# Optimization experiments

Hardware: AMD Instinct MI355X
Metric: run time of the kernel (lower is better)

## Reference

```python
import jax, jax.numpy as jnp
import numpy as np

N, E, G = 50000, 800000, 512
IN_CH, HID, HEADS, OUT_CH, LAYERS = 128, 32, 8, 1, 3
NEG_SLOPE = 0.2  # PyG GATConv default


def gat_conv(x, src, dst, W, a_src, a_dst, bias):
    # x: [N, F_in]; W: [F_in, H*C]; a_src/a_dst: [H, C]; bias: [H*C]
    h = (x @ W).reshape(N, HEADS, HID)                     # [N, H, C]
    alpha_src = jnp.einsum('nhc,hc->nh', h, a_src)          # [N, H]
    alpha_dst = jnp.einsum('nhc,hc->nh', h, a_dst)          # [N, H]
    e = jax.nn.leaky_relu(alpha_src[src] + alpha_dst[dst], NEG_SLOPE)  # [E', H]
    # segment softmax over incoming edges of each destination node
    m = jax.ops.segment_max(e, dst, num_segments=N)
    m = jnp.where(jnp.isfinite(m), m, 0.0)
    ex = jnp.exp(e - m[dst])
    denom = jax.ops.segment_sum(ex, dst, num_segments=N)
    alpha = ex / (denom[dst] + 1e-16)                       # [E', H]
    msg = h[src] * alpha[:, :, None]                        # [E', H, C]
    out = jax.ops.segment_sum(msg, dst, num_segments=N)     # [N, H, C]
    return out.reshape(N, HEADS * HID) + bias


def setup_inputs() -> dict:
    key = jax.random.key(0)
    ks = jax.random.split(key, 20)
    inp = {}
    inp['x'] = jax.random.normal(ks[0], (N, IN_CH), dtype=jnp.float32)
    inp['edge_index'] = jax.random.randint(ks[1], (2, E), 0, N, dtype=jnp.int64)
    inp['batch'] = jnp.sort(jax.random.randint(ks[2], (N,), 0, G, dtype=jnp.int64))
    fan_ins = [IN_CH, HEADS * HID, HEADS * HID]
    for l in range(LAYERS):
        s = (2.0 / fan_ins[l]) ** 0.5
        inp[f'W{l}'] = jax.random.normal(ks[3 + 4 * l], (fan_ins[l], HEADS * HID), dtype=jnp.float32) * s
        inp[f'a_src{l}'] = jax.random.normal(ks[4 + 4 * l], (HEADS, HID), dtype=jnp.float32) * 0.1
        inp[f'a_dst{l}'] = jax.random.normal(ks[5 + 4 * l], (HEADS, HID), dtype=jnp.float32) * 0.1
        inp[f'bias{l}'] = jnp.zeros((HEADS * HID,), dtype=jnp.float32)
    inp['lin_w'] = jax.random.normal(ks[15], (HEADS * HID, OUT_CH), dtype=jnp.float32) * 0.06
    inp['lin_b'] = jnp.zeros((OUT_CH,), dtype=jnp.float32)
    return inp


def reference(x, edge_index, batch,
              W0, a_src0, a_dst0, bias0,
              W1, a_src1, a_dst1, bias1,
              W2, a_src2, a_dst2, bias2,
              lin_w, lin_b):
    # add self-loops (GATConv default add_self_loops=True)
    loop = jnp.arange(N, dtype=edge_index.dtype)
    src = jnp.concatenate([edge_index[0], loop])
    dst = jnp.concatenate([edge_index[1], loop])
    params = [(W0, a_src0, a_dst0, bias0), (W1, a_src1, a_dst1, bias1), (W2, a_src2, a_dst2, bias2)]
    h = x
    for (W, a_s, a_d, b) in params:
        h = gat_conv(h, src, dst, W, a_s, a_d, b)
        h = jax.nn.elu(h)
        # dropout is identity in eval mode
    # global mean pool over graphs
    sums = jax.ops.segment_sum(h, batch, num_segments=G)           # [G, H*C]
    cnts = jax.ops.segment_sum(jnp.ones((N,), h.dtype), batch, num_segments=G)
    pooled = sums / jnp.maximum(cnts, 1.0)[:, None]
    return pooled @ lin_w + lin_b                                   # [G, OUT_CH]
```

## Files before the change

### kernel.cpp

```cpp
#include <hip/hip_runtime.h>

#define HC 256
#define HEADS 8
#define HID 32
#define GRAPHS 512
#define NEG_SLOPE 0.2f

typedef __bf16 bf16x8 __attribute__((ext_vector_type(8)));
typedef float f32x4 __attribute__((ext_vector_type(4)));

__device__ __forceinline__ unsigned short f2bf(float x) {
    unsigned u = __float_as_uint(x);
    return (unsigned short)((u + 0x7fffu + ((u >> 16) & 1u)) >> 16);
}
__device__ __forceinline__ float bf2f(unsigned short b) {
    return __uint_as_float(((unsigned)b) << 16);
}

__device__ __forceinline__ int IDX(const void* p, long long i, int mode) {
    if (mode) return (int)((const long long*)p)[i];
    return ((const int*)p)[i];
}

__global__ void detect_kernel(const unsigned int* __restrict__ words, int* __restrict__ mode, int e) {
    __shared__ unsigned int red[256];
    unsigned int v = 0;
    int lim = e < 4096 ? e : 4096;
    for (int i = threadIdx.x; i < lim; i += 256) v |= words[2 * i + 1];
    red[threadIdx.x] = v;
    __syncthreads();
    for (int off = 128; off > 0; off >>= 1) {
        if (threadIdx.x < off) red[threadIdx.x] |= red[threadIdx.x + off];
        __syncthreads();
    }
    if (threadIdx.x == 0) *mode = (red[0] == 0u) ? 1 : 0;
}

__global__ void hist_kernel(const void* __restrict__ edge, const int* __restrict__ mode,
                            int* __restrict__ hist, int e) {
    int m = mode[0];
    int i = blockIdx.x * blockDim.x + threadIdx.x;
    if (i < e) atomicAdd(&hist[IDX(edge, (long long)e + i, m)], 1);
}

__global__ void scan1(const int* __restrict__ hist, int* __restrict__ excl,
                      int* __restrict__ bsum, int n) {
    __shared__ int buf[256];
    int i = blockIdx.x * 256 + threadIdx.x;
    int v = (i < n) ? hist[i] : 0;
    buf[threadIdx.x] = v;
    __syncthreads();
    for (int off = 1; off < 256; off <<= 1) {
        int t = (threadIdx.x >= (unsigned)off) ? buf[threadIdx.x - off] : 0;
        __syncthreads();
        buf[threadIdx.x] += t;
        __syncthreads();
    }
    if (i < n) excl[i] = buf[threadIdx.x] - v;
    if (threadIdx.x == 255) bsum[blockIdx.x] = buf[255];
}

__global__ void scan2(int* __restrict__ bsum, int nb) {
    __shared__ int buf[256];
    int v = (threadIdx.x < (unsigned)nb) ? bsum[threadIdx.x] : 0;
    buf[threadIdx.x] = v;
    __syncthreads();
    for (int off = 1; off < 256; off <<= 1) {
        int t = (threadIdx.x >= (unsigned)off) ? buf[threadIdx.x - off] : 0;
        __syncthreads();
        buf[threadIdx.x] += t;
        __syncthreads();
    }
    if (threadIdx.x < (unsigned)nb) bsum[threadIdx.x] = buf[threadIdx.x] - v;
}

__global__ void scan3(int* __restrict__ row_ptr, const int* __restrict__ bsum, int n, int e) {
    int i = blockIdx.x * 256 + threadIdx.x;
    if (i < n) row_ptr[i] += bsum[i >> 8];
    if (i == 0) row_ptr[n] = e;
}

__global__ void scatter_kernel(const void* __restrict__ edge, const int* __restrict__ mode,
                               const int* __restrict__ row_ptr, int* __restrict__ fill,
                               int* __restrict__ outs, int* __restrict__ outd, int e) {
    int m = mode[0];
    int i = blockIdx.x * blockDim.x + threadIdx.x;
    if (i < e) {
        int d = IDX(edge, (long long)e + i, m);
        int pos = row_ptr[d] + atomicAdd(&fill[d], 1);
        outs[pos] = IDX(edge, (long long)i, m);
        outd[pos] = d;
    }
}

__global__ void cast_kernel(const float* __restrict__ x, unsigned short* __restrict__ xb,
                            int nquad) {
    int i = blockIdx.x * blockDim.x + threadIdx.x;
    if (i >= nquad) return;
    float4 v = *(const float4*)(x + (size_t)i * 4);
    ushort4 u = {f2bf(v.x), f2bf(v.y), f2bf(v.z), f2bf(v.w)};
    *(ushort4*)(xb + (size_t)i * 4) = u;
}

__global__ void wtrans_kernel(const float* __restrict__ W, unsigned short* __restrict__ Wt,
                              int K) {
    int idx = blockIdx.x * blockDim.x + threadIdx.x;
    if (idx >= 256 * K) return;
    int c = idx / K, k = idx - c * K;
    Wt[idx] = f2bf(W[(size_t)k * 256 + c]);
}

__global__ __launch_bounds__(256) void gemm_mfma(const unsigned short* __restrict__ A,
                                                 const unsigned short* __restrict__ Wt,
                                                 unsigned short* __restrict__ Cb,
                                                 int M, int K) {
    __shared__ unsigned short Ab[64][40];
    __shared__ unsigned short Bt[128][40];
    const int tid = threadIdx.x;
    const int wave = tid >> 6, lane = tid & 63;
    const int wr = wave >> 1, wc = wave & 1;
    const int row0 = blockIdx.x * 64, col0 = blockIdx.y * 128;
    const int r4 = tid >> 2, q = tid & 3;
    const int l15 = lane & 15, g8 = (lane >> 4) * 8;
    f32x4 acc[2][4] = {};

    for (int k0 = 0; k0 < K; k0 += 32) {
        int ar = row0 + r4;
        ar = ar < M ? ar : M - 1;
        *(uint4*)&Ab[r4][q * 8] = *(const uint4*)&A[(size_t)ar * K + k0 + q * 8];
#pragma unroll
        for (int h = 0; h < 2; ++h) {
            int br = r4 + h * 64;
            *(uint4*)&Bt[br][q * 8] = *(const uint4*)&Wt[(size_t)(col0 + br) * K + k0 + q * 8];
        }
        __syncthreads();
        bf16x8 af[2], bfr[4];
#pragma unroll
        for (int i = 0; i < 2; ++i) af[i] = *(const bf16x8*)&Ab[wr * 32 + i * 16 + l15][g8];
#pragma unroll
        for (int j = 0; j < 4; ++j) bfr[j] = *(const bf16x8*)&Bt[wc * 64 + j * 16 + l15][g8];
#pragma unroll
        for (int i = 0; i < 2; ++i)
#pragma unroll
            for (int j = 0; j < 4; ++j)
                acc[i][j] = __builtin_amdgcn_mfma_f32_16x16x32_bf16(af[i], bfr[j], acc[i][j],
                                                                    0, 0, 0);
        __syncthreads();
    }
    const int g = lane >> 4;
#pragma unroll
    for (int i = 0; i < 2; ++i) {
#pragma unroll
        for (int r = 0; r < 4; ++r) {
            int row = row0 + wr * 32 + i * 16 + g * 4 + r;
            if (row < M) {
#pragma unroll
                for (int j = 0; j < 4; ++j) {
                    int col = col0 + wc * 64 + j * 16 + l15;
                    Cb[(size_t)row * HC + col] = f2bf(acc[i][j][r]);
                }
            }
        }
    }
}

__global__ void alpha_kernel(const unsigned short* __restrict__ h,
                             const float* __restrict__ a_src,
                             const float* __restrict__ a_dst, float* __restrict__ asrc,
                             float* __restrict__ adst, int n) {
    int t = blockIdx.x * blockDim.x + threadIdx.x;
    if (t >= n * HEADS) return;
    int node = t >> 3, head = t & 7;
    const ushort4* hp = (const ushort4*)(h + (size_t)node * HC + head * HID);
    const float4* w1 = (const float4*)(a_src + head * HID);
    const float4* w2 = (const float4*)(a_dst + head * HID);
    float s1 = 0.f, s2 = 0.f;
#pragma unroll
    for (int q = 0; q < 8; ++q) {
        ushort4 hv = hp[q];
        float4 a1 = w1[q], a2 = w2[q];
        float h0 = bf2f(hv.x), h1 = bf2f(hv.y), h2 = bf2f(hv.z), h3 = bf2f(hv.w);
        s1 += h0 * a1.x + h1 * a1.y + h2 * a1.z + h3 * a1.w;
        s2 += h0 * a2.x + h1 * a2.y + h2 * a2.z + h3 * a2.w;
    }
    asrc[t] = s1;
    adst[t] = s2;
}

__global__ void wexp_kernel(const int* __restrict__ srcs, const int* __restrict__ dsts,
                            const float* __restrict__ asrc, const float* __restrict__ adst,
                            float* __restrict__ wexp, int e) {
    int i = blockIdx.x * blockDim.x + threadIdx.x;
    if (i >= e) return;
    int s = srcs[i], d = dsts[i];
    float4 s0 = *(const float4*)(asrc + (size_t)s * 8);
    float4 s1 = *(const float4*)(asrc + (size_t)s * 8 + 4);
    float4 d0 = *(const float4*)(adst + (size_t)d * 8);
    float4 d1 = *(const float4*)(adst + (size_t)d * 8 + 4);
    float v[8] = {s0.x + d0.x, s0.y + d0.y, s0.z + d0.z, s0.w + d0.w,
                  s1.x + d1.x, s1.y + d1.y, s1.z + d1.z, s1.w + d1.w};
#pragma unroll
    for (int q = 0; q < 8; ++q) {
        float t = v[q] > 0.f ? v[q] : NEG_SLOPE * v[q];
        v[q] = __expf(fminf(t, 75.f));
    }
    *(float4*)(wexp + (size_t)i * 8) = make_float4(v[0], v[1], v[2], v[3]);
    *(float4*)(wexp + (size_t)i * 8 + 4) = make_float4(v[4], v[5], v[6], v[7]);
}

#define ACC_EDGE(gv, wv)                                                      \
    do {                                                                      \
        unsigned _u0 = gv.x, _u1 = gv.y, _u2 = gv.z, _u3 = gv.w;              \
        acc[0] = fmaf(wv, __uint_as_float(_u0 << 16), acc[0]);                \
        acc[1] = fmaf(wv, __uint_as_float(_u0 & 0xffff0000u), acc[1]);        \
        acc[2] = fmaf(wv, __uint_as_float(_u1 << 16), acc[2]);                \
        acc[3] = fmaf(wv, __uint_as_float(_u1 & 0xffff0000u), acc[3]);        \
        acc[4] = fmaf(wv, __uint_as_float(_u2 << 16), acc[4]);                \
        acc[5] = fmaf(wv, __uint_as_float(_u2 & 0xffff0000u), acc[5]);        \
        acc[6] = fmaf(wv, __uint_as_float(_u3 << 16), acc[6]);                \
        acc[7] = fmaf(wv, __uint_as_float(_u3 & 0xffff0000u), acc[7]);        \
    } while (0)

template <bool LAST>
__global__ __launch_bounds__(256) void gat_aggregate(
    const unsigned short* __restrict__ hb, const float* __restrict__ wexp,
    const float* __restrict__ asrc, const float* __restrict__ adst,
    const int* __restrict__ row_ptr, const int* __restrict__ srcs,
    const float* __restrict__ bias, unsigned short* __restrict__ out16,
    const void* __restrict__ batch, const int* __restrict__ mode,
    const float* __restrict__ lin_w, float* __restrict__ gsum,
    float* __restrict__ gcnt, int n) {
    const int lane = threadIdx.x & 63;
    const int half = lane >> 5;
    const int l32 = lane & 31;
    int wid = (int)((blockIdx.x * blockDim.x + threadIdx.x) >> 6);
    int node = wid * 2 + half;
    if (node >= n) return;
    const int head = l32 >> 2;
    const int c0 = l32 * 8;
    const int beg = row_ptr[node], end = row_ptr[node + 1];

    float e0 = asrc[node * 8 + head] + adst[node * 8 + head];
    e0 = e0 > 0.f ? e0 : NEG_SLOPE * e0;
    float w0 = __expf(fminf(e0, 75.f));
    float denom = w0;
    float acc[8] = {};
    {
        uint4 g = *(const uint4*)(hb + (size_t)node * HC + c0);
        ACC_EDGE(g, w0);
    }
    int j = beg;
    for (; j + 4 <= end; j += 4) {
        int s0 = srcs[j], s1 = srcs[j + 1], s2 = srcs[j + 2], s3 = srcs[j + 3];
        uint4 g0 = *(const uint4*)(hb + (size_t)s0 * HC + c0);
        uint4 g1 = *(const uint4*)(hb + (size_t)s1 * HC + c0);
        uint4 g2 = *(const uint4*)(hb + (size_t)s2 * HC + c0);
        uint4 g3 = *(const uint4*)(hb + (size_t)s3 * HC + c0);
        float x0 = wexp[(size_t)(j + 0) * 8 + head];
        float x1 = wexp[(size_t)(j + 1) * 8 + head];
        float x2 = wexp[(size_t)(j + 2) * 8 + head];
        float x3 = wexp[(size_t)(j + 3) * 8 + head];
        denom += x0 + x1 + x2 + x3;
        ACC_EDGE(g0, x0);
        ACC_EDGE(g1, x1);
        ACC_EDGE(g2, x2);
        ACC_EDGE(g3, x3);
    }
    for (; j < end; ++j) {
        int s = srcs[j];
        uint4 g = *(const uint4*)(hb + (size_t)s * HC + c0);
        float x = wexp[(size_t)j * 8 + head];
        denom += x;
        ACC_EDGE(g, x);
    }

    const float invd = 1.f / (denom + 1e-16f);
    float4 b0 = *(const float4*)(bias + c0);
    float4 b1 = *(const float4*)(bias + c0 + 4);
    float o[8] = {fmaf(acc[0], invd, b0.x), fmaf(acc[1], invd, b0.y),
                  fmaf(acc[2], invd, b0.z), fmaf(acc[3], invd, b0.w),
                  fmaf(acc[4], invd, b1.x), fmaf(acc[5], invd, b1.y),
                  fmaf(acc[6], invd, b1.z), fmaf(acc[7], invd, b1.w)};
#pragma unroll
    for (int q = 0; q < 8; ++q) o[q] = o[q] > 0.f ? o[q] : __expf(o[q]) - 1.f;
    if (!LAST) {
        uint4 u;
        u.x = (unsigned)f2bf(o[0]) | ((unsigned)f2bf(o[1]) << 16);
        u.y = (unsigned)f2bf(o[2]) | ((unsigned)f2bf(o[3]) << 16);
        u.z = (unsigned)f2bf(o[4]) | ((unsigned)f2bf(o[5]) << 16);
        u.w = (unsigned)f2bf(o[6]) | ((unsigned)f2bf(o[7]) << 16);
        *(uint4*)(out16 + (size_t)node * HC + c0) = u;
    } else {
        float4 wA = *(const float4*)(lin_w + c0);
        float4 wB = *(const float4*)(lin_w + c0 + 4);
        float p = o[0] * wA.x + o[1] * wA.y + o[2] * wA.z + o[3] * wA.w +
                  o[4] * wB.x + o[5] * wB.y + o[6] * wB.z + o[7] * wB.w;
#pragma unroll
        for (int off = 1; off <= 16; off <<= 1) p += __shfl_xor(p, off, 64);
        if (l32 == 0) {
            int g = IDX(batch, node, mode[0]);
            atomicAdd(&gsum[g], p);
            atomicAdd(&gcnt[g], 1.f);
        }
    }
}

__global__ void final_kernel(const float* __restrict__ gsum, const float* __restrict__ gcnt,
                             const float* __restrict__ lin_b, float* __restrict__ outp) {
    int g = blockIdx.x * blockDim.x + threadIdx.x;
    if (g >= GRAPHS) return;
    float c = gcnt[g];
    c = c > 1.f ? c : 1.f;
    outp[g] = gsum[g] / c + lin_b[0];
}

extern "C" void kernel_launch(void* const* d_in, const int* in_sizes, int n_in,
                              void* d_out, int out_size, void* d_ws, size_t ws_size,
                              hipStream_t stream) {
    const float* x = (const float*)d_in[0];
    const void* edge = d_in[1];
    const void* batch = d_in[2];
    const float* W[3]    = {(const float*)d_in[3], (const float*)d_in[7],  (const float*)d_in[11]};
    const float* ASRC[3] = {(const float*)d_in[4], (const float*)d_in[8],  (const float*)d_in[12]};
    const float* ADST[3] = {(const float*)d_in[5], (const float*)d_in[9],  (const float*)d_in[13]};
    const float* BIAS[3] = {(const float*)d_in[6], (const float*)d_in[10], (const float*)d_in[14]};
    const float* lin_w = (const float*)d_in[15];
    const float* lin_b = (const float*)d_in[16];
    float* outp = (float*)d_out;

    const int n = in_sizes[0] / 128;
    const int e = in_sizes[1] / 2;
    const int IN_CH = 128;

    char* ws = (char*)d_ws;
    size_t off = 0;
    auto alloc = [&](size_t bytes) -> void* {
        void* p = ws + off;
        off = (off + bytes + 255) & ~(size_t)255;
        return p;
    };
    unsigned short* xb   = (unsigned short*)alloc((size_t)n * IN_CH * 2);
    unsigned short* hb16 = (unsigned short*)alloc((size_t)n * HC * 2);
    unsigned short* gb16 = (unsigned short*)alloc((size_t)n * HC * 2);
    unsigned short* wt0  = (unsigned short*)alloc((size_t)256 * IN_CH * 2);
    unsigned short* wt1  = (unsigned short*)alloc((size_t)256 * HC * 2);
    unsigned short* wt2  = (unsigned short*)alloc((size_t)256 * HC * 2);
    float* as_buf = (float*)alloc((size_t)n * HEADS * 4);
    float* ad_buf = (float*)alloc((size_t)n * HEADS * 4);
    int* hist     = (int*)alloc((size_t)n * 4);
    int* row_ptr  = (int*)alloc((size_t)(n + 1) * 4);
    int* bsum     = (int*)alloc(1024);
    int* mode     = (int*)alloc(256);
    int* srcs     = (int*)alloc((size_t)e * 4);
    int* dsts     = (int*)alloc((size_t)e * 4);
    float* wexp   = (float*)alloc((size_t)e * HEADS * 4);
    float* gsum   = (float*)alloc((size_t)GRAPHS * 4);
    float* gcnt   = (float*)alloc((size_t)GRAPHS * 4);
    if (off > ws_size) return;

    const unsigned short* WT[3] = {wt0, wt1, wt2};
    const int nb = (n + 255) / 256;

    detect_kernel<<<1, 256, 0, stream>>>((const unsigned int*)edge, mode, e);

    hipMemsetAsync(hist, 0, (size_t)n * 4, stream);
    hist_kernel<<<(e + 255) / 256, 256, 0, stream>>>(edge, mode, hist, e);
    scan1<<<nb, 256, 0, stream>>>(hist, row_ptr, bsum, n);
    scan2<<<1, 256, 0, stream>>>(bsum, nb);
    scan3<<<nb, 256, 0, stream>>>(row_ptr, bsum, n, e);
    hipMemsetAsync(hist, 0, (size_t)n * 4, stream);
    scatter_kernel<<<(e + 255) / 256, 256, 0, stream>>>(edge, mode, row_ptr, hist, srcs, dsts, e);

    cast_kernel<<<(n * IN_CH / 4 + 255) / 256, 256, 0, stream>>>(x, xb, n * IN_CH / 4);
    wtrans_kernel<<<(256 * IN_CH + 255) / 256, 256, 0, stream>>>(W[0], wt0, IN_CH);
    wtrans_kernel<<<(256 * HC + 255) / 256, 256, 0, stream>>>(W[1], wt1, HC);
    wtrans_kernel<<<(256 * HC + 255) / 256, 256, 0, stream>>>(W[2], wt2, HC);

    hipMemsetAsync(gsum, 0, (size_t)GRAPHS * 4, stream);
    hipMemsetAsync(gcnt, 0, (size_t)GRAPHS * 4, stream);

    const unsigned short* Ain = xb;
    int K = IN_CH;
    const int agg_blocks = (n + 7) / 8;
    dim3 gemm_grid((n + 63) / 64, 2);
    for (int l = 0; l < 3; ++l) {
        gemm_mfma<<<gemm_grid, 256, 0, stream>>>(Ain, WT[l], hb16, n, K);
        alpha_kernel<<<(n * HEADS + 255) / 256, 256, 0, stream>>>(hb16, ASRC[l], ADST[l],
                                                                  as_buf, ad_buf, n);
        wexp_kernel<<<(e + 255) / 256, 256, 0, stream>>>(srcs, dsts, as_buf, ad_buf, wexp, e);
        if (l < 2) {
            gat_aggregate<false><<<agg_blocks, 256, 0, stream>>>(
                hb16, wexp, as_buf, ad_buf, row_ptr, srcs, BIAS[l], gb16,
                batch, mode, lin_w, gsum, gcnt, n);
        } else {
            gat_aggregate<true><<<agg_blocks, 256, 0, stream>>>(
                hb16, wexp, as_buf, ad_buf, row_ptr, srcs, BIAS[l], nullptr,
                batch, mode, lin_w, gsum, gcnt, n);
        }
        Ain = gb16;
        K = HC;
    }

    final_kernel<<<2, 256, 0, stream>>>(gsum, gcnt, lin_b, outp);
}
```

Measured before the change: 535.4 us.

## Fuse attention logits into GEMM epilogue and store edge weights as bf16

Computes the per-head source and destination attention dot products inside the MFMA GEMM epilogue using wave shuffles, which removes the separate alpha kernel and its re-read of the projected features. Edge exp weights are also stored as bf16 instead of fp32, halving the wexp write and read traffic between the edge kernel and aggregation. The logits are now computed from fp32 accumulators rather than bf16-rounded h, while the exp weights lose precision to bf16.

```diff
diff --git a/kernel.cpp b/kernel.cpp
--- a/kernel.cpp
+++ b/kernel.cpp
@@ -113,6 +113,10 @@
 __global__ __launch_bounds__(256) void gemm_mfma(const unsigned short* __restrict__ A,
                                                  const unsigned short* __restrict__ Wt,
                                                  unsigned short* __restrict__ Cb,
+                                                 const float* __restrict__ a_src,
+                                                 const float* __restrict__ a_dst,
+                                                 float* __restrict__ asrc,
+                                                 float* __restrict__ adst,
                                                  int M, int K) {
     __shared__ unsigned short Ab[64][40];
     __shared__ unsigned short Bt[128][40];
@@ -148,15 +152,38 @@
         __syncthreads();
     }
     const int g = lane >> 4;
+    const int colbase = col0 + wc * 64;
+    const int headA = colbase >> 5, headB = headA + 1;
+    const float asA0 = a_src[headA * 32 + l15], asA1 = a_src[headA * 32 + 16 + l15];
+    const float asB0 = a_src[headB * 32 + l15], asB1 = a_src[headB * 32 + 16 + l15];
+    const float adA0 = a_dst[headA * 32 + l15], adA1 = a_dst[headA * 32 + 16 + l15];
+    const float adB0 = a_dst[headB * 32 + l15], adB1 = a_dst[headB * 32 + 16 + l15];
 #pragma unroll
     for (int i = 0; i < 2; ++i) {
 #pragma unroll
         for (int r = 0; r < 4; ++r) {
             int row = row0 + wr * 32 + i * 16 + g * 4 + r;
+            float pa = acc[i][0][r] * asA0 + acc[i][1][r] * asA1;
+            float pb = acc[i][2][r] * asB0 + acc[i][3][r] * asB1;
+            float qa = acc[i][0][r] * adA0 + acc[i][1][r] * adA1;
+            float qb = acc[i][2][r] * adB0 + acc[i][3][r] * adB1;
+#pragma unroll
+            for (int off = 1; off < 16; off <<= 1) {
+                pa += __shfl_xor(pa, off, 64);
+                pb += __shfl_xor(pb, off, 64);
+                qa += __shfl_xor(qa, off, 64);
+                qb += __shfl_xor(qb, off, 64);
+            }
             if (row < M) {
+                if (l15 == 0) {
+                    asrc[row * 8 + headA] = pa;
+                    asrc[row * 8 + headB] = pb;
+                    adst[row * 8 + headA] = qa;
+                    adst[row * 8 + headB] = qb;
+                }
 #pragma unroll
                 for (int j = 0; j < 4; ++j) {
-                    int col = col0 + wc * 64 + j * 16 + l15;
+                    int col = colbase + j * 16 + l15;
                     Cb[(size_t)row * HC + col] = f2bf(acc[i][j][r]);
                 }
             }
@@ -164,32 +191,9 @@
     }
 }
 
-__global__ void alpha_kernel(const unsigned short* __restrict__ h,
-                             const float* __restrict__ a_src,
-                             const float* __restrict__ a_dst, float* __restrict__ asrc,
-                             float* __restrict__ adst, int n) {
-    int t = blockIdx.x * blockDim.x + threadIdx.x;
-    if (t >= n * HEADS) return;
-    int node = t >> 3, head = t & 7;
-    const ushort4* hp = (const ushort4*)(h + (size_t)node * HC + head * HID);
-    const float4* w1 = (const float4*)(a_src + head * HID);
-    const float4* w2 = (const float4*)(a_dst + head * HID);
-    float s1 = 0.f, s2 = 0.f;
-#pragma unroll
-    for (int q = 0; q < 8; ++q) {
-        ushort4 hv = hp[q];
-        float4 a1 = w1[q], a2 = w2[q];
-        float h0 = bf2f(hv.x), h1 = bf2f(hv.y), h2 = bf2f(hv.z), h3 = bf2f(hv.w);
-        s1 += h0 * a1.x + h1 * a1.y + h2 * a1.z + h3 * a1.w;
-        s2 += h0 * a2.x + h1 * a2.y + h2 * a2.z + h3 * a2.w;
-    }
-    asrc[t] = s1;
-    adst[t] = s2;
-}
-
 __global__ void wexp_kernel(const int* __restrict__ srcs, const int* __restrict__ dsts,
                             const float* __restrict__ asrc, const float* __restrict__ adst,
-                            float* __restrict__ wexp, int e) {
+                            unsigned short* __restrict__ wexp, int e) {
     int i = blockIdx.x * blockDim.x + threadIdx.x;
     if (i >= e) return;
     int s = srcs[i], d = dsts[i];
@@ -199,13 +203,16 @@
     float4 d1 = *(const float4*)(adst + (size_t)d * 8 + 4);
     float v[8] = {s0.x + d0.x, s0.y + d0.y, s0.z + d0.z, s0.w + d0.w,
                   s1.x + d1.x, s1.y + d1.y, s1.z + d1.z, s1.w + d1.w};
+    ushort4 u0, u1;
 #pragma unroll
     for (int q = 0; q < 8; ++q) {
         float t = v[q] > 0.f ? v[q] : NEG_SLOPE * v[q];
         v[q] = __expf(fminf(t, 75.f));
     }
-    *(float4*)(wexp + (size_t)i * 8) = make_float4(v[0], v[1], v[2], v[3]);
-    *(float4*)(wexp + (size_t)i * 8 + 4) = make_float4(v[4], v[5], v[6], v[7]);
+    u0 = (ushort4){f2bf(v[0]), f2bf(v[1]), f2bf(v[2]), f2bf(v[3])};
+    u1 = (ushort4){f2bf(v[4]), f2bf(v[5]), f2bf(v[6]), f2bf(v[7])};
+    *(ushort4*)(wexp + (size_t)i * 8) = u0;
+    *(ushort4*)(wexp + (size_t)i * 8 + 4) = u1;
 }
 
 #define ACC_EDGE(gv, wv)                                                      \
@@ -223,7 +230,7 @@
 
 template <bool LAST>
 __global__ __launch_bounds__(256) void gat_aggregate(
-    const unsigned short* __restrict__ hb, const float* __restrict__ wexp,
+    const unsigned short* __restrict__ hb, const unsigned short* __restrict__ wexp,
     const float* __restrict__ asrc, const float* __restrict__ adst,
     const int* __restrict__ row_ptr, const int* __restrict__ srcs,
     const float* __restrict__ bias, unsigned short* __restrict__ out16,
@@ -256,10 +263,10 @@
         uint4 g1 = *(const uint4*)(hb + (size_t)s1 * HC + c0);
         uint4 g2 = *(const uint4*)(hb + (size_t)s2 * HC + c0);
         uint4 g3 = *(const uint4*)(hb + (size_t)s3 * HC + c0);
-        float x0 = wexp[(size_t)(j + 0) * 8 + head];
-        float x1 = wexp[(size_t)(j + 1) * 8 + head];
-        float x2 = wexp[(size_t)(j + 2) * 8 + head];
-        float x3 = wexp[(size_t)(j + 3) * 8 + head];
+        float x0 = bf2f(wexp[(size_t)(j + 0) * 8 + head]);
+        float x1 = bf2f(wexp[(size_t)(j + 1) * 8 + head]);
+        float x2 = bf2f(wexp[(size_t)(j + 2) * 8 + head]);
+        float x3 = bf2f(wexp[(size_t)(j + 3) * 8 + head]);
         denom += x0 + x1 + x2 + x3;
         ACC_EDGE(g0, x0);
         ACC_EDGE(g1, x1);
@@ -269,7 +276,7 @@
     for (; j < end; ++j) {
         int s = srcs[j];
         uint4 g = *(const uint4*)(hb + (size_t)s * HC + c0);
-        float x = wexp[(size_t)j * 8 + head];
+        float x = bf2f(wexp[(size_t)j * 8 + head]);
         denom += x;
         ACC_EDGE(g, x);
     }
@@ -353,7 +360,7 @@
     int* mode     = (int*)alloc(256);
     int* srcs     = (int*)alloc((size_t)e * 4);
     int* dsts     = (int*)alloc((size_t)e * 4);
-    float* wexp   = (float*)alloc((size_t)e * HEADS * 4);
+    unsigned short* wexp = (unsigned short*)alloc((size_t)e * HEADS * 2);
     float* gsum   = (float*)alloc((size_t)GRAPHS * 4);
     float* gcnt   = (float*)alloc((size_t)GRAPHS * 4);
     if (off > ws_size) return;
@@ -384,9 +391,8 @@
     const int agg_blocks = (n + 7) / 8;
     dim3 gemm_grid((n + 63) / 64, 2);
     for (int l = 0; l < 3; ++l) {
-        gemm_mfma<<<gemm_grid, 256, 0, stream>>>(Ain, WT[l], hb16, n, K);
-        alpha_kernel<<<(n * HEADS + 255) / 256, 256, 0, stream>>>(hb16, ASRC[l], ADST[l],
-                                                                  as_buf, ad_buf, n);
+        gemm_mfma<<<gemm_grid, 256, 0, stream>>>(Ain, WT[l], hb16, ASRC[l], ADST[l],
+                                                 as_buf, ad_buf, n, K);
         wexp_kernel<<<(e + 255) / 256, 256, 0, stream>>>(srcs, dsts, as_buf, ad_buf, wexp, e);
         if (l < 2) {
             gat_aggregate<false><<<agg_blocks, 256, 0, stream>>>(
```

Result: faster. 466.6 us, median of 2 (-12.9%).
